# Kernel optimization log

Hardware: AMD Instinct MI355X
Metric: run time of the kernel (lower is better)

## Reference

```python
import jax, jax.numpy as jnp
import numpy as np

B, N, D = 4, 1024, 2048
H_Q, H_KV = 16, 4
D_HEAD = D // H_Q            # 128
GROUPS = H_Q // H_KV         # 4
ROPE_BASE = 10000.0


def rms_norm(x, w, eps):
    # normalize over last dim (d_head), learnable scale w
    ms = jnp.mean(jnp.square(x), axis=-1, keepdims=True)
    return x * jax.lax.rsqrt(ms + eps) * w


def apply_rope(t, pos):
    # t: (B, H, N, d). Half-split RoPE rotation.
    d = t.shape[-1]
    inv_freq = 1.0 / (ROPE_BASE ** (jnp.arange(0, d, 2, dtype=jnp.float32) / d))  # (d/2,)
    ang = pos.astype(jnp.float32)[:, None] * inv_freq[None, :]                     # (N, d/2)
    cos, sin = jnp.cos(ang), jnp.sin(ang)                                          # (N, d/2)
    t1, t2 = t[..., : d // 2], t[..., d // 2 :]
    return jnp.concatenate([t1 * cos - t2 * sin, t2 * cos + t1 * sin], axis=-1)


def setup_inputs() -> dict:
    key = jax.random.key(0)
    ks = jax.random.split(key, 4)
    x = jax.random.normal(ks[0], (B, N, D), dtype=jnp.float32)
    w_qkv = jax.random.normal(ks[1], (D_HEAD * (H_Q + 2 * H_KV), D), dtype=jnp.float32) * (D ** -0.5)
    w_out = jax.random.normal(ks[2], (D, D), dtype=jnp.float32) * (D ** -0.5)
    q_norm_w = jnp.ones((D_HEAD,), dtype=jnp.float32)
    k_norm_w = jnp.ones((D_HEAD,), dtype=jnp.float32)
    mask = jnp.triu(jnp.ones((N, N), dtype=bool), k=1)  # True = masked (causal)
    pos = jnp.arange(N, dtype=jnp.int64) if jax.config.jax_enable_x64 else jnp.arange(N, dtype=jnp.int32)
    return {"x": x, "mask": mask, "pos": pos, "w_qkv": w_qkv, "w_out": w_out,
            "q_norm_w": q_norm_w, "k_norm_w": k_norm_w}


def reference(x, mask, pos, w_qkv, w_out, q_norm_w, k_norm_w):
    eps = jnp.finfo(x.dtype).eps
    scale = D_HEAD ** -0.5
    # fused QKV projection, split into heads
    qkv = jnp.einsum('bnd,ed->bne', x, w_qkv)                       # (B, N, (Hq+2Hkv)*d)
    qkv = qkv.reshape(B, N, H_Q + 2 * H_KV, D_HEAD).transpose(0, 2, 1, 3)
    q, k, v = jnp.split(qkv, [H_Q, H_Q + H_KV], axis=1)             # (B,Hq,N,d),(B,Hkv,N,d)x2
    # qk RMSNorm
    q = rms_norm(q, q_norm_w, eps)
    k = rms_norm(k, k_norm_w, eps)
    # RoPE
    q = apply_rope(q, pos)
    k = apply_rope(k, pos)
    # GQA: repeat kv heads across groups
    k = jnp.repeat(k, GROUPS, axis=1)                               # (B, Hq, N, d)
    v = jnp.repeat(v, GROUPS, axis=1)
    # manual attention (non-flash path)
    scores = jnp.einsum('bhqd,bhkd->bhqk', q, k) * scale            # (B, Hq, N, N)
    scores = jnp.where(mask, -jnp.inf, scores)
    attn = jax.nn.softmax(scores, axis=-1)
    y = jnp.einsum('bhqk,bhkd->bhqd', attn, v)                      # (B, Hq, N, d)
    y = y.transpose(0, 2, 1, 3).reshape(B, N, D)
    return jnp.einsum('bnd,ed->bne', y, w_out)                      # out_proj
```

## Files before the change

### kernel.cpp

```cpp
#include <hip/hip_runtime.h>
#include <cstdint>
#include <cstddef>

#define B_   4
#define N_   1024
#define D_   2048
#define HQ_  16
#define HKV_ 4
#define DH_  128
#define E_   3072

#define SCALE_ 0.08838834764831845

typedef __attribute__((ext_vector_type(8))) short frag16;
typedef __attribute__((ext_vector_type(4))) float fragf4;
#define MFMA16(a, b, c) __builtin_amdgcn_mfma_f32_16x16x32_bf16(a, b, c, 0, 0, 0)

__device__ __forceinline__ short f2bf(float f) {
  union { float f; uint32_t u; } a; a.f = f;
  uint32_t r = (a.u + 0x7fffu + ((a.u >> 16) & 1u)) >> 16;
  return (short)r;
}
__device__ __forceinline__ short f2bf_t(float f) {
  union { float f; uint32_t u; } a; a.f = f;
  return (short)(a.u >> 16);
}
__device__ __forceinline__ void async_copy16(const void* g, void* l) {
  __builtin_amdgcn_global_load_lds(
      (const __attribute__((address_space(1))) void*)g,
      (__attribute__((address_space(3))) void*)l, 16, 0, 0);
}

__global__ __launch_bounds__(256) void f2bf3_kernel(
    const float* __restrict__ s0, short* __restrict__ d0, int b0,
    const float* __restrict__ s1, short* __restrict__ d1, int b1,
    const float* __restrict__ s2, short* __restrict__ d2) {
  int bx = blockIdx.x;
  const float* s; short* d;
  if (bx < b0)           { s = s0; d = d0; }
  else if (bx < b0 + b1) { s = s1; d = d1; bx -= b0; }
  else                   { s = s2; d = d2; bx -= b0 + b1; }
  const int i = (bx * 256 + threadIdx.x) * 8;
  float4 a = *(const float4*)(s + i);
  float4 b = *(const float4*)(s + i + 4);
  union { frag16 f; short sh[8]; } u;
  u.sh[0] = f2bf(a.x); u.sh[1] = f2bf(a.y); u.sh[2] = f2bf(a.z); u.sh[3] = f2bf(a.w);
  u.sh[4] = f2bf(b.x); u.sh[5] = f2bf(b.y); u.sh[6] = f2bf(b.z); u.sh[7] = f2bf(b.w);
  *(frag16*)(d + i) = u.f;
}

template <typename OutT>
__global__ __launch_bounds__(256) void gemm_mfma(const short* __restrict__ A,
                                                 const short* __restrict__ Wt,
                                                 OutT* __restrict__ C,
                                                 int Nc, int K, int ncpx) {
  __shared__ __align__(16) short As[128][64];
  __shared__ __align__(16) short Bs[128][64];

  const int bid = blockIdx.x;
  const int xcd = bid & 7, j = bid >> 3;
  const int m0 = (j & 31) * 128;
  const int n0 = (xcd * ncpx + (j >> 5)) * 128;

  const int tid = threadIdx.x;
  const int lane = tid & 63;
  const int w = tid >> 6;
  const int ln = lane & 15, g = lane >> 4;
  const int wm = (w >> 1) * 64, wn = (w & 1) * 64;

  const int srow = lane >> 3;
  const int schunk = ((lane & 7) ^ srow) * 8;
  const int l7 = ln & 7;

  fragf4 acc[4][4];
#pragma unroll
  for (int i = 0; i < 4; ++i)
#pragma unroll
    for (int jj = 0; jj < 4; ++jj) acc[i][jj] = (fragf4){0.f, 0.f, 0.f, 0.f};

  for (int k0 = 0; k0 < K; k0 += 64) {
    __syncthreads();
#pragma unroll
    for (int i = 0; i < 4; ++i) {
      const int rbase = w * 32 + i * 8;
      const int r = rbase + srow;
      async_copy16(A  + (size_t)(m0 + r) * K + k0 + schunk, &As[rbase][0]);
      async_copy16(Wt + (size_t)(n0 + r) * K + k0 + schunk, &Bs[rbase][0]);
    }
    __syncthreads();

    frag16 af[2][4], bf[2][4];
#pragma unroll
    for (int c = 0; c < 2; ++c) {
      const int pc = (((c << 2) | g) ^ l7) * 8;
#pragma unroll
      for (int t = 0; t < 4; ++t) {
        af[c][t] = *(const frag16*)&As[wm + t * 16 + ln][pc];
        bf[c][t] = *(const frag16*)&Bs[wn + t * 16 + ln][pc];
      }
    }
#pragma unroll
    for (int c = 0; c < 2; ++c)
#pragma unroll
      for (int i = 0; i < 4; ++i)
#pragma unroll
        for (int jj = 0; jj < 4; ++jj)
          acc[i][jj] = MFMA16(af[c][i], bf[c][jj], acc[i][jj]);
  }

#pragma unroll
  for (int i = 0; i < 4; ++i) {
#pragma unroll
    for (int jj = 0; jj < 4; ++jj) {
#pragma unroll
      for (int r = 0; r < 4; ++r) {
        const size_t idx = (size_t)(m0 + wm + i * 16 + 4 * g + r) * Nc +
                           (n0 + wn + jj * 16 + ln);
        if constexpr (sizeof(OutT) == 2) C[idx] = f2bf(acc[i][jj][r]);
        else                             C[idx] = acc[i][jj][r];
      }
    }
  }
}

__global__ __launch_bounds__(256) void normrope_vt(short* __restrict__ qkvb,
                                                   short* __restrict__ vtg,
                                                   const int* __restrict__ pos,
                                                   const float* __restrict__ qw,
                                                   const float* __restrict__ kw,
                                                   int nrB) {
  __shared__ short T[128 * 72];
  const int tid = threadIdx.x;

  if ((int)blockIdx.x < nrB) {
    const int gid = blockIdx.x * 256 + tid;
    const int lane = gid & 63;
    const int wid = gid >> 6;
    const int hh = wid % (HQ_ + HKV_);
    const int n  = (wid / (HQ_ + HKV_)) % N_;
    const int b  = wid / ((HQ_ + HKV_) * N_);

    int eoff; const float* w;
    if (hh < HQ_) { eoff = hh * DH_;              w = qw; }
    else          { eoff = D_ + (hh - HQ_) * DH_; w = kw; }

    short* base = qkvb + ((size_t)b * N_ + n) * E_ + eoff;
    union { uint32_t u; float f; } c1, c2;
    c1.u = ((uint32_t)(uint16_t)base[lane]) << 16;
    c2.u = ((uint32_t)(uint16_t)base[64 + lane]) << 16;
    float t1 = c1.f, t2 = c2.f;

    float ss = t1 * t1 + t2 * t2;
#pragma unroll
    for (int off = 32; off; off >>= 1) ss += __shfl_xor(ss, off);
    const float r = rsqrtf(ss * (1.0f / 128.0f) + 1.1920928955078125e-07f);
    t1 = t1 * r * w[lane];
    t2 = t2 * r * w[64 + lane];

    const float invf = (float)exp2(-(double)lane * 0.20762050593046014);
    const float ang = (float)pos[n] * invf;
    const float c = cosf(ang), s = sinf(ang);
    base[lane]      = f2bf(t1 * c - t2 * s);
    base[64 + lane] = f2bf(t2 * c + t1 * s);
  } else {
    const int idx = blockIdx.x - nrB;
    const int n0 = (idx & 15) * 64, kh = (idx >> 4) & 3, b = idx >> 6;
    {
      const int r = tid & 63, dc = (tid >> 6) * 32;
      const short* src = qkvb + ((size_t)b * N_ + n0 + r) * E_ + 2560 + kh * DH_ + dc;
      union { frag16 f; short s[8]; } u;
#pragma unroll
      for (int i = 0; i < 4; ++i) {
        u.f = *(const frag16*)(src + 8 * i);
#pragma unroll
        for (int jj = 0; jj < 8; ++jj) T[(dc + 8 * i + jj) * 72 + r] = u.s[jj];
      }
    }
    __syncthreads();
    {
      const int d = tid & 127, e = tid >> 7;
      short* dst = vtg + ((size_t)(b * HKV_ + kh) * DH_ + d) * N_ + n0 + e * 32;
#pragma unroll
      for (int i = 0; i < 4; ++i)
        *(frag16*)(dst + 8 * i) = *(const frag16*)&T[d * 72 + e * 32 + 8 * i];
    }
  }
}

__global__ __launch_bounds__(256) void attn_mfma(const short* __restrict__ qkvb,
                                                 const short* __restrict__ vtg,
                                                 short* __restrict__ yb) {
  const int bx = blockIdx.x;
  const int qt = 63 - (bx >> 4);
  const int id = bx & 15;
  const int kh = id & 3, b = id >> 2;
  const int q0 = qt * 16;

  __shared__ __align__(16) short lds_[22600];
  const int VT0 = 8704, PS0 = 17992;

  const int tid = threadIdx.x;
  const int lane = tid & 63;
  const int w = tid >> 6;
  const int ln = lane & 15, g = lane >> 4, g8 = g * 8;
  const int h = kh * 4 + w;

  const short* qb = qkvb + (size_t)b * N_ * E_ + h * DH_;
  const short* kb = qkvb + (size_t)b * N_ * E_ + D_ + kh * DH_;
  const short* vt = vtg + (size_t)(b * HKV_ + kh) * DH_ * N_;

  if (tid < 64) lds_[VT0 + 128 * 72 + tid] = (short)0x3F80;

  frag16 qf[4];
  {
    const short* qrow = qb + (size_t)(q0 + ln) * E_ + g8;
#pragma unroll
    for (int c = 0; c < 4; ++c) qf[c] = *(const frag16*)(qrow + c * 32);
  }

  fragf4 o[8], ol = (fragf4){0.f, 0.f, 0.f, 0.f};
#pragma unroll
  for (int dt = 0; dt < 8; ++dt) o[dt] = (fragf4){0.f, 0.f, 0.f, 0.f};

  const float SC2 = (float)(SCALE_ * 1.4426950408889634);
  const float MB2 = (float)(12.0 * 1.4426950408889634);

  const int ntiles = qt / 4 + 1;
  for (int kt = 0; kt < ntiles; ++kt) {
    const int kbase = kt * 64;
    __syncthreads();
    {
      const int r = tid & 63, c = (tid >> 6) * 32;
      const short* src = kb + (size_t)(kbase + r) * E_ + c;
#pragma unroll
      for (int i = 0; i < 4; ++i)
        *(frag16*)&lds_[r * 136 + c + 8 * i] = *(const frag16*)(src + 8 * i);
    }
    {
      const int d = tid & 127, e = tid >> 7;
      const short* src = vt + (size_t)d * N_ + kbase + e * 32;
#pragma unroll
      for (int i = 0; i < 4; ++i)
        *(frag16*)&lds_[VT0 + d * 72 + e * 32 + 8 * i] = *(const frag16*)(src + 8 * i);
    }
    __syncthreads();

    fragf4 s[4];
#pragma unroll
    for (int st = 0; st < 4; ++st) s[st] = (fragf4){0.f, 0.f, 0.f, 0.f};
#pragma unroll
    for (int c = 0; c < 4; ++c) {
      frag16 qc = qf[c];
#pragma unroll
      for (int st = 0; st < 4; ++st) {
        frag16 kf = *(const frag16*)&lds_[(st * 16 + ln) * 136 + c * 32 + g8];
        s[st] = MFMA16(qc, kf, s[st]);
      }
    }

    const bool full = (kbase + 63) <= q0;
#pragma unroll
    for (int st = 0; st < 4; ++st) {
      const int kg = kbase + st * 16 + ln;
#pragma unroll
      for (int r2 = 0; r2 < 4; ++r2) {
        float sv = s[st][r2];
        if (!full && kg > q0 + 4 * g + r2) sv = -1.0e30f;
        const float p = exp2f(fmaf(sv, SC2, -MB2));
        lds_[PS0 + (w * 16 + 4 * g + r2) * 72 + st * 16 + ln] = f2bf_t(p);
      }
    }

    frag16 pf0 = *(const frag16*)&lds_[PS0 + (w * 16 + ln) * 72 + g8];
    frag16 pf1 = *(const frag16*)&lds_[PS0 + (w * 16 + ln) * 72 + 32 + g8];
#pragma unroll
    for (int dt = 0; dt < 8; ++dt) {
      frag16 v0 = *(const frag16*)&lds_[VT0 + (dt * 16 + ln) * 72 + g8];
      frag16 v1 = *(const frag16*)&lds_[VT0 + (dt * 16 + ln) * 72 + 32 + g8];
      o[dt] = MFMA16(pf0, v0, o[dt]);
      o[dt] = MFMA16(pf1, v1, o[dt]);
    }
    {
      frag16 vl0 = *(const frag16*)&lds_[VT0 + (128 + ln) * 72 + g8];
      frag16 vl1 = *(const frag16*)&lds_[VT0 + (128 + ln) * 72 + 32 + g8];
      ol = MFMA16(pf0, vl0, ol);
      ol = MFMA16(pf1, vl1, ol);
    }
  }

#pragma unroll
  for (int r2 = 0; r2 < 4; ++r2) {
    const float lv = __shfl(ol[r2], lane & 48);
    const float inv = 1.0f / lv;
    short* yrow = yb + ((size_t)b * N_ + q0 + 4 * g + r2) * D_ + h * DH_;
#pragma unroll
    for (int dt = 0; dt < 8; ++dt) yrow[dt * 16 + ln] = f2bf(o[dt][r2] * inv);
  }
}

extern "C" void kernel_launch(void* const* d_in, const int* in_sizes, int n_in,
                              void* d_out, int out_size, void* d_ws, size_t ws_size,
                              hipStream_t stream) {
  const float* x     = (const float*)d_in[0];
  const int*   pos   = (const int*)d_in[2];
  const float* w_qkv = (const float*)d_in[3];
  const float* w_out = (const float*)d_in[4];
  const float* qw    = (const float*)d_in[5];
  const float* kw    = (const float*)d_in[6];
  float* out = (float*)d_out;

  short* qkvb = (short*)d_ws;
  short* yb   = qkvb + (size_t)B_ * N_ * E_;
  short* xb   = yb   + (size_t)B_ * N_ * D_;
  short* wqb  = xb   + (size_t)B_ * N_ * D_;
  short* wob  = wqb  + (size_t)E_ * D_;
  short* vtg  = xb;

  const int nx = B_ * N_ * D_, nwq = E_ * D_, nwo = D_ * D_;
  const int bx_ = nx / 2048, bwq = nwq / 2048, bwo = nwo / 2048;
  f2bf3_kernel<<<bx_ + bwq + bwo, 256, 0, stream>>>(
      x, xb, bx_, w_qkv, wqb, bwq, w_out, wob);

  gemm_mfma<short><<<768, 256, 0, stream>>>(xb, wqb, qkvb, E_, D_, 3);

  const int nrB = (B_ * N_ * (HQ_ + HKV_) * 64) / 256;
  normrope_vt<<<nrB + 256, 256, 0, stream>>>(qkvb, vtg, pos, qw, kw, nrB);

  attn_mfma<<<1024, 256, 0, stream>>>(qkvb, vtg, yb);

  gemm_mfma<float><<<512, 256, 0, stream>>>(yb, wob, out, D_, D_, 2);
}
```

Measured before the change: 304.1 us.

## Process two query tiles per wave in attention and swizzle LDS layout

Each attention block now handles 32 query rows per head (two 16-row tiles per wave), so every K/V tile loaded into LDS serves twice as many MFMAs, and the grid is halved. The K and V^T LDS buffers switch from padded strides to an XOR-swizzled layout to avoid bank conflicts. The row-sum is computed by MFMA against a register vector of ones instead of an extra LDS row. The cost is more registers per thread (doubled accumulators), which may reduce occupancy, and fewer blocks for the causal load imbalance to spread across.

```diff
diff --git a/kernel.cpp b/kernel.cpp
--- a/kernel.cpp
+++ b/kernel.cpp
@@ -191,110 +191,141 @@
                                                  const short* __restrict__ vtg,
                                                  short* __restrict__ yb) {
   const int bx = blockIdx.x;
-  const int qt = 63 - (bx >> 4);
+  const int qt2 = 31 - (bx >> 4);
   const int id = bx & 15;
   const int kh = id & 3, b = id >> 2;
-  const int q0 = qt * 16;
-
-  __shared__ __align__(16) short lds_[22600];
-  const int VT0 = 8704, PS0 = 17992;
+  const int q0 = qt2 * 32;
+
+  __shared__ __align__(16) short lds_[27648];
+  const int VT0 = 8192, PS0 = 16384;
 
   const int tid = threadIdx.x;
   const int lane = tid & 63;
   const int w = tid >> 6;
-  const int ln = lane & 15, g = lane >> 4, g8 = g * 8;
+  const int ln = lane & 15, g = lane >> 4, g8 = g * 8, l7 = ln & 7;
   const int h = kh * 4 + w;
+  const int psw = PS0 + w * 2816;
 
   const short* qb = qkvb + (size_t)b * N_ * E_ + h * DH_;
   const short* kb = qkvb + (size_t)b * N_ * E_ + D_ + kh * DH_;
   const short* vt = vtg + (size_t)(b * HKV_ + kh) * DH_ * N_;
 
-  if (tid < 64) lds_[VT0 + 128 * 72 + tid] = (short)0x3F80;
-
-  frag16 qf[4];
-  {
-    const short* qrow = qb + (size_t)(q0 + ln) * E_ + g8;
-#pragma unroll
-    for (int c = 0; c < 4; ++c) qf[c] = *(const frag16*)(qrow + c * 32);
-  }
-
-  fragf4 o[8], ol = (fragf4){0.f, 0.f, 0.f, 0.f};
-#pragma unroll
-  for (int dt = 0; dt < 8; ++dt) o[dt] = (fragf4){0.f, 0.f, 0.f, 0.f};
+  frag16 qf[2][4];
+#pragma unroll
+  for (int t = 0; t < 2; ++t) {
+    const short* qrow = qb + (size_t)(q0 + 16 * t + ln) * E_ + g8;
+#pragma unroll
+    for (int c = 0; c < 4; ++c) qf[t][c] = *(const frag16*)(qrow + c * 32);
+  }
+
+  frag16 ones;
+#pragma unroll
+  for (int j = 0; j < 8; ++j) ones[j] = (short)0x3F80;
+
+  fragf4 o[2][8], ol[2];
+#pragma unroll
+  for (int t = 0; t < 2; ++t) {
+    ol[t] = (fragf4){0.f, 0.f, 0.f, 0.f};
+#pragma unroll
+    for (int dt = 0; dt < 8; ++dt) o[t][dt] = (fragf4){0.f, 0.f, 0.f, 0.f};
+  }
 
   const float SC2 = (float)(SCALE_ * 1.4426950408889634);
   const float MB2 = (float)(12.0 * 1.4426950408889634);
 
-  const int ntiles = qt / 4 + 1;
+  const int krow = tid >> 2, kgrp = tid & 3;
+  const int vrow = tid >> 1, vgrp = tid & 1;
+
+  const int ntiles = (q0 + 95) >> 6;
   for (int kt = 0; kt < ntiles; ++kt) {
     const int kbase = kt * 64;
     __syncthreads();
     {
-      const int r = tid & 63, c = (tid >> 6) * 32;
-      const short* src = kb + (size_t)(kbase + r) * E_ + c;
-#pragma unroll
-      for (int i = 0; i < 4; ++i)
-        *(frag16*)&lds_[r * 136 + c + 8 * i] = *(const frag16*)(src + 8 * i);
+      const short* src = kb + (size_t)(kbase + krow) * E_ + kgrp * 32;
+      const int r7 = krow & 7;
+#pragma unroll
+      for (int i = 0; i < 4; ++i) {
+        const int lc = kgrp * 4 + i;
+        *(frag16*)&lds_[krow * 128 + (lc ^ r7) * 8] = *(const frag16*)(src + i * 8);
+      }
     }
     {
-      const int d = tid & 127, e = tid >> 7;
-      const short* src = vt + (size_t)d * N_ + kbase + e * 32;
-#pragma unroll
-      for (int i = 0; i < 4; ++i)
-        *(frag16*)&lds_[VT0 + d * 72 + e * 32 + 8 * i] = *(const frag16*)(src + 8 * i);
-    }
-    __syncthreads();
-
-    fragf4 s[4];
-#pragma unroll
-    for (int st = 0; st < 4; ++st) s[st] = (fragf4){0.f, 0.f, 0.f, 0.f};
+      const short* src = vt + (size_t)vrow * N_ + kbase + vgrp * 32;
+      const int r7 = vrow & 7;
+#pragma unroll
+      for (int i = 0; i < 4; ++i) {
+        const int lc = vgrp * 4 + i;
+        *(frag16*)&lds_[VT0 + vrow * 64 + (lc ^ r7) * 8] = *(const frag16*)(src + i * 8);
+      }
+    }
+    __syncthreads();
+
+    fragf4 s[2][4];
+#pragma unroll
+    for (int t = 0; t < 2; ++t)
+#pragma unroll
+      for (int st = 0; st < 4; ++st) s[t][st] = (fragf4){0.f, 0.f, 0.f, 0.f};
 #pragma unroll
     for (int c = 0; c < 4; ++c) {
-      frag16 qc = qf[c];
+      const int pc = ((c * 4 + g) ^ l7) * 8;
 #pragma unroll
       for (int st = 0; st < 4; ++st) {
-        frag16 kf = *(const frag16*)&lds_[(st * 16 + ln) * 136 + c * 32 + g8];
-        s[st] = MFMA16(qc, kf, s[st]);
-      }
-    }
-
-    const bool full = (kbase + 63) <= q0;
-#pragma unroll
-    for (int st = 0; st < 4; ++st) {
-      const int kg = kbase + st * 16 + ln;
-#pragma unroll
-      for (int r2 = 0; r2 < 4; ++r2) {
-        float sv = s[st][r2];
-        if (!full && kg > q0 + 4 * g + r2) sv = -1.0e30f;
-        const float p = exp2f(fmaf(sv, SC2, -MB2));
-        lds_[PS0 + (w * 16 + 4 * g + r2) * 72 + st * 16 + ln] = f2bf_t(p);
-      }
-    }
-
-    frag16 pf0 = *(const frag16*)&lds_[PS0 + (w * 16 + ln) * 72 + g8];
-    frag16 pf1 = *(const frag16*)&lds_[PS0 + (w * 16 + ln) * 72 + 32 + g8];
+        frag16 kf = *(const frag16*)&lds_[(st * 16 + ln) * 128 + pc];
+        s[0][st] = MFMA16(qf[0][c], kf, s[0][st]);
+        s[1][st] = MFMA16(qf[1][c], kf, s[1][st]);
+      }
+    }
+
+#pragma unroll
+    for (int t = 0; t < 2; ++t) {
+      const int qbase = q0 + 16 * t;
+      const bool full = (kbase + 63) <= qbase;
+#pragma unroll
+      for (int st = 0; st < 4; ++st) {
+        const int kg = kbase + st * 16 + ln;
+        const int po = psw + (st >> 1) * 48 + (st & 1) * 16 + ln;
+#pragma unroll
+        for (int r2 = 0; r2 < 4; ++r2) {
+          float sv = s[t][st][r2];
+          if (!full && kg > qbase + 4 * g + r2) sv = -1.0e30f;
+          const float p = exp2f(fmaf(sv, SC2, -MB2));
+          lds_[po + (16 * t + 4 * g + r2) * 88] = f2bf_t(p);
+        }
+      }
+    }
+
+    frag16 pf[2][2];
+#pragma unroll
+    for (int t = 0; t < 2; ++t)
+#pragma unroll
+      for (int hh = 0; hh < 2; ++hh)
+        pf[t][hh] = *(const frag16*)&lds_[psw + (16 * t + ln) * 88 + hh * 48 + g8];
 #pragma unroll
     for (int dt = 0; dt < 8; ++dt) {
-      frag16 v0 = *(const frag16*)&lds_[VT0 + (dt * 16 + ln) * 72 + g8];
-      frag16 v1 = *(const frag16*)&lds_[VT0 + (dt * 16 + ln) * 72 + 32 + g8];
-      o[dt] = MFMA16(pf0, v0, o[dt]);
-      o[dt] = MFMA16(pf1, v1, o[dt]);
-    }
-    {
-      frag16 vl0 = *(const frag16*)&lds_[VT0 + (128 + ln) * 72 + g8];
-      frag16 vl1 = *(const frag16*)&lds_[VT0 + (128 + ln) * 72 + 32 + g8];
-      ol = MFMA16(pf0, vl0, ol);
-      ol = MFMA16(pf1, vl1, ol);
-    }
-  }
-
-#pragma unroll
-  for (int r2 = 0; r2 < 4; ++r2) {
-    const float lv = __shfl(ol[r2], lane & 48);
-    const float inv = 1.0f / lv;
-    short* yrow = yb + ((size_t)b * N_ + q0 + 4 * g + r2) * D_ + h * DH_;
-#pragma unroll
-    for (int dt = 0; dt < 8; ++dt) yrow[dt * 16 + ln] = f2bf(o[dt][r2] * inv);
+#pragma unroll
+      for (int hh = 0; hh < 2; ++hh) {
+        const int pv = ((hh * 4 + g) ^ l7) * 8;
+        frag16 vf = *(const frag16*)&lds_[VT0 + (dt * 16 + ln) * 64 + pv];
+        o[0][dt] = MFMA16(pf[0][hh], vf, o[0][dt]);
+        o[1][dt] = MFMA16(pf[1][hh], vf, o[1][dt]);
+      }
+    }
+#pragma unroll
+    for (int t = 0; t < 2; ++t) {
+      ol[t] = MFMA16(pf[t][0], ones, ol[t]);
+      ol[t] = MFMA16(pf[t][1], ones, ol[t]);
+    }
+  }
+
+#pragma unroll
+  for (int t = 0; t < 2; ++t) {
+#pragma unroll
+    for (int r2 = 0; r2 < 4; ++r2) {
+      const float inv = 1.0f / ol[t][r2];
+      short* yrow = yb + ((size_t)b * N_ + q0 + 16 * t + 4 * g + r2) * D_ + h * DH_;
+#pragma unroll
+      for (int dt = 0; dt < 8; ++dt) yrow[dt * 16 + ln] = f2bf(o[t][dt][r2] * inv);
+    }
   }
 }
 
@@ -326,7 +357,7 @@
   const int nrB = (B_ * N_ * (HQ_ + HKV_) * 64) / 256;
   normrope_vt<<<nrB + 256, 256, 0, stream>>>(qkvb, vtg, pos, qw, kw, nrB);
 
-  attn_mfma<<<1024, 256, 0, stream>>>(qkvb, vtg, yb);
+  attn_mfma<<<512, 256, 0, stream>>>(qkvb, vtg, yb);
 
   gemm_mfma<float><<<512, 256, 0, stream>>>(yb, wob, out, D_, D_, 2);
 }
```

Result: slower. 313.1 us (+3.0%).
